# Performance work log

Hardware: AMD Instinct MI355X
Metric: run time of the kernel (lower is better)

The kernel has to match this reference:

```python
import math
import jax, jax.numpy as jnp
import numpy as np

L = 2          # num_layers
B = 2          # micro batch
S = 2048       # seq_length
H = 1024       # hidden_size
NH = 16        # num_attention_heads
DH = 64        # kv_channels (head dim)
FF = 4096      # ffn_hidden_size
EPS = 1e-5
STD = 0.0048


def setup_inputs() -> dict:
    key = jax.random.key(0)
    ks = jax.random.split(key, 12)
    out_std = STD / math.sqrt(2.0 * L)
    # ALiBi slopes for NH=16 (power of 2)
    start = 2.0 ** (-2.0 ** (-(math.log2(NH) - 3)))
    slopes = np.array([start * start ** i for i in range(NH)], dtype=np.float32)
    alibi = slopes[None, :, None, None] * np.arange(S, dtype=np.float32)[None, None, None, :]
    alibi = jnp.asarray(np.broadcast_to(alibi, (B, NH, 1, S)))  # [B, NH, 1, S]
    return {
        "hidden_states": jax.random.normal(ks[0], (B, S, H), jnp.float32),
        "alibi": alibi,
        "qkv_w": jax.random.normal(ks[1], (L, 3 * NH * DH, H), jnp.float32) * STD,
        "qkv_b": jnp.zeros((L, 3 * NH * DH), jnp.float32),
        "dense_w": jax.random.normal(ks[2], (L, H, NH * DH), jnp.float32) * out_std,
        "dense_b": jnp.zeros((L, H), jnp.float32),
        "mlp_w1": jax.random.normal(ks[3], (L, FF, H), jnp.float32) * STD,
        "mlp_b1": jnp.zeros((L, FF), jnp.float32),
        "mlp_w2": jax.random.normal(ks[4], (L, H, FF), jnp.float32) * out_std,
        "mlp_b2": jnp.zeros((L, H), jnp.float32),
        "ln1_w": jnp.ones((L, H), jnp.float32),
        "ln1_b": jnp.zeros((L, H), jnp.float32),
        "ln2_w": jnp.ones((L, H), jnp.float32),
        "ln2_b": jnp.zeros((L, H), jnp.float32),
    }


def _layernorm(x, w, b):
    mu = jnp.mean(x, axis=-1, keepdims=True)
    var = jnp.mean(jnp.square(x - mu), axis=-1, keepdims=True)
    return (x - mu) * jax.lax.rsqrt(var + EPS) * w + b


def _layer(x, alibi, causal, layer_number, qkv_w, qkv_b, dense_w, dense_b,
           mlp_w1, mlp_b1, mlp_w2, mlp_b2, ln1_w, ln1_b, ln2_w, ln2_b):
    # --- attention ---
    h = _layernorm(x, ln1_w, ln1_b)
    qkv = h @ qkv_w.T + qkv_b                       # [B, S, 3*NH*DH]
    q, k, v = jnp.split(qkv, 3, axis=-1)
    q = q.reshape(B, S, NH, DH).transpose(0, 2, 1, 3)  # [B, NH, S, DH]
    k = k.reshape(B, S, NH, DH).transpose(0, 2, 1, 3)
    v = v.reshape(B, S, NH, DH).transpose(0, 2, 1, 3)
    norm_factor = math.sqrt(DH) * layer_number
    beta = 1.0 / layer_number
    alpha = 1.0 / norm_factor
    scores = beta * alibi + alpha * jnp.einsum("bhqd,bhkd->bhqk", q, k)
    # ScaleMaskSoftmax: scale by layer_number, causal mask fill -10000, softmax
    scores = scores * layer_number
    scores = jnp.where(causal, scores, jnp.float32(-10000.0))
    probs = jax.nn.softmax(scores, axis=-1)
    ctx = jnp.einsum("bhqk,bhkd->bhqd", probs, v)   # [B, NH, S, DH]
    ctx = ctx.transpose(0, 2, 1, 3).reshape(B, S, NH * DH)
    attn_out = ctx @ dense_w.T + dense_b
    x = x + attn_out
    # --- MLP ---
    h2 = _layernorm(x, ln2_w, ln2_b)
    m = jax.nn.gelu(h2 @ mlp_w1.T + mlp_b1, approximate=False)
    m = m @ mlp_w2.T + mlp_b2
    return x + m


def reference(hidden_states, alibi, qkv_w, qkv_b, dense_w, dense_b,
              mlp_w1, mlp_b1, mlp_w2, mlp_b2, ln1_w, ln1_b, ln2_w, ln2_b):
    causal = jnp.tril(jnp.ones((S, S), dtype=bool))[None, None]  # [1,1,S,S]
    x = hidden_states
    for l in range(L):
        x = _layer(x, alibi, causal, l + 1,
                   qkv_w[l], qkv_b[l], dense_w[l], dense_b[l],
                   mlp_w1[l], mlp_b1[l], mlp_w2[l], mlp_b2[l],
                   ln1_w[l], ln1_b[l], ln2_w[l], ln2_b[l])
    return x
```

## Files before the change

kernel.cpp:

```cpp
#include <hip/hip_runtime.h>
#include <cstdint>
#include <cmath>

#define SS 2048
#define HH 1024

typedef __bf16 bf16_t;
typedef __bf16 bf16x8 __attribute__((ext_vector_type(8)));
typedef __bf16 bf16x4 __attribute__((ext_vector_type(4)));
typedef float  f32x4  __attribute__((ext_vector_type(4)));

union U32P { unsigned u; bf16_t h[2]; };

__device__ __forceinline__ void async_load16(const void* g, void* l) {
  __builtin_amdgcn_global_load_lds(
      (__attribute__((address_space(1))) void*)(g),
      (__attribute__((address_space(3))) void*)(l), 16, 0, 0);
}

__device__ __forceinline__ void bar_lds() {
  asm volatile("s_waitcnt lgkmcnt(0)" ::: "memory");
  __builtin_amdgcn_s_barrier();
}

__global__ __launch_bounds__(256) void cvt_kernel(const float* __restrict__ in,
                                                  bf16_t* __restrict__ out) {
  size_t i = (size_t)blockIdx.x * 256 + threadIdx.x;
  f32x4 v = ((const f32x4*)in)[i];
  bf16x4 o;
  o[0] = (bf16_t)v[0]; o[1] = (bf16_t)v[1]; o[2] = (bf16_t)v[2]; o[3] = (bf16_t)v[3];
  ((bf16x4*)out)[i] = o;
}

__global__ __launch_bounds__(256) void ln_kernel(const float* __restrict__ x,
                                                 const float* __restrict__ w,
                                                 const float* __restrict__ b,
                                                 bf16_t* __restrict__ out) {
  const int row = blockIdx.x;
  const int tid = threadIdx.x;
  const f32x4 v = ((const f32x4*)(x + (size_t)row * HH))[tid];
  float s  = v[0] + v[1] + v[2] + v[3];
  float s2 = v[0]*v[0] + v[1]*v[1] + v[2]*v[2] + v[3]*v[3];
#pragma unroll
  for (int o = 1; o < 64; o <<= 1) { s += __shfl_xor(s, o); s2 += __shfl_xor(s2, o); }
  __shared__ float r1[4], r2[4];
  if ((tid & 63) == 0) { r1[tid >> 6] = s; r2[tid >> 6] = s2; }
  __syncthreads();
  float ts  = r1[0] + r1[1] + r1[2] + r1[3];
  float ts2 = r2[0] + r2[1] + r2[2] + r2[3];
  float mu  = ts * (1.0f / HH);
  float var = ts2 * (1.0f / HH) - mu * mu;
  float rstd = rsqrtf(var + 1e-5f);
  f32x4 wv = ((const f32x4*)w)[tid];
  f32x4 bv = ((const f32x4*)b)[tid];
  bf16x4 o;
#pragma unroll
  for (int j = 0; j < 4; ++j) o[j] = (bf16_t)((v[j] - mu) * rstd * wv[j] + bv[j]);
  ((bf16x4*)(out + (size_t)row * HH))[tid] = o;
}

__device__ __forceinline__ float gelu_f(float x) {
  return 0.5f * x * (1.0f + erff(x * 0.70710678118654752f));
}

__global__ __launch_bounds__(256) void fuse_add(float* __restrict__ x,
                                                const bf16_t* __restrict__ p0,
                                                const bf16_t* __restrict__ p1,
                                                const float* __restrict__ bias) {
  size_t i = (size_t)blockIdx.x * 256 + threadIdx.x;
  f32x4 xv = ((f32x4*)x)[i];
  bf16x4 a = ((const bf16x4*)p0)[i];
  bf16x4 b4 = ((const bf16x4*)p1)[i];
  f32x4 bv = ((const f32x4*)bias)[i & 255];
#pragma unroll
  for (int j = 0; j < 4; ++j) xv[j] += (float)a[j] + (float)b4[j] + bv[j];
  ((f32x4*)x)[i] = xv;
}

template <int EPI>
__global__ __launch_bounds__(256) void gemm_bt(const bf16_t* __restrict__ A,
                                               const bf16_t* __restrict__ W,
                                               const float* __restrict__ bias,
                                               bf16_t* __restrict__ outb,
                                               int M, int N, int K) {
  __shared__ __align__(16) bf16_t As[128 * 64];
  __shared__ __align__(16) bf16_t Bs[128 * 64];
  const int tid = threadIdx.x;
  const int w = tid >> 6, lane = tid & 63;
  const int m16 = lane & 15, quad = lane >> 4;
  const int wm = w & 1, wn = w >> 1;
  const int n0 = blockIdx.x * 128, m0 = blockIdx.y * 128;

  f32x4 acc[4][4];
#pragma unroll
  for (int i = 0; i < 4; ++i)
#pragma unroll
    for (int j = 0; j < 4; ++j) acc[i][j] = (f32x4){0.f, 0.f, 0.f, 0.f};

  int rowi[4], gci[4];
#pragma unroll
  for (int i = 0; i < 4; ++i) {
    int p = (w * 4 + i) * 64 + lane;
    rowi[i] = p >> 3;
    gci[i] = ((lane & 7) ^ (rowi[i] & 7)) * 8;
  }

  for (int kt = 0; kt < K; kt += 64) {
    __syncthreads();
#pragma unroll
    for (int i = 0; i < 4; ++i) {
      async_load16(A + (size_t)(m0 + rowi[i]) * K + kt + gci[i], &As[(w * 4 + i) * 512]);
      async_load16(W + (size_t)(n0 + rowi[i]) * K + kt + gci[i], &Bs[(w * 4 + i) * 512]);
    }
    __syncthreads();
#pragma unroll
    for (int kk = 0; kk < 2; ++kk) {
      bf16x8 af[4], bfv[4];
#pragma unroll
      for (int mi = 0; mi < 4; ++mi) {
        int row = wm * 64 + mi * 16 + m16;
        int cpos = (kk * 4 + quad) ^ (row & 7);
        af[mi] = *(const bf16x8*)&As[row * 64 + cpos * 8];
      }
#pragma unroll
      for (int ni = 0; ni < 4; ++ni) {
        int row = wn * 64 + ni * 16 + m16;
        int cpos = (kk * 4 + quad) ^ (row & 7);
        bfv[ni] = *(const bf16x8*)&Bs[row * 64 + cpos * 8];
      }
#pragma unroll
      for (int mi = 0; mi < 4; ++mi)
#pragma unroll
        for (int ni = 0; ni < 4; ++ni)
          acc[mi][ni] = __builtin_amdgcn_mfma_f32_16x16x32_bf16(af[mi], bfv[ni],
                                                                acc[mi][ni], 0, 0, 0);
    }
  }

#pragma unroll
  for (int ni = 0; ni < 4; ++ni) {
    int col = n0 + wn * 64 + ni * 16 + m16;
    float bv = bias[col];
#pragma unroll
    for (int mi = 0; mi < 4; ++mi) {
      int rowb = m0 + wm * 64 + mi * 16 + quad * 4;
#pragma unroll
      for (int r = 0; r < 4; ++r) {
        size_t idx = (size_t)(rowb + r) * N + col;
        float v = acc[mi][ni][r] + bv;
        if constexpr (EPI == 1) v = gelu_f(v);
        outb[idx] = (bf16_t)v;
      }
    }
  }
}

__global__ __launch_bounds__(256) void gemm_sk2(const bf16_t* __restrict__ A,
                                                const bf16_t* __restrict__ W,
                                                bf16_t* __restrict__ p0,
                                                bf16_t* __restrict__ p1,
                                                int M, int N, int K) {
  __shared__ __align__(16) bf16_t As[128 * 64];
  __shared__ __align__(16) bf16_t Bs[128 * 64];
  const int tid = threadIdx.x;
  const int w = tid >> 6, lane = tid & 63;
  const int m16 = lane & 15, quad = lane >> 4;
  const int wm = w & 1, wn = w >> 1;
  const int n0 = blockIdx.x * 128, m0 = blockIdx.y * 128;
  const int z = blockIdx.z;
  const int kbeg = z * (K >> 1), kend = kbeg + (K >> 1);
  bf16_t* outb = z ? p1 : p0;

  f32x4 acc[4][4];
#pragma unroll
  for (int i = 0; i < 4; ++i)
#pragma unroll
    for (int j = 0; j < 4; ++j) acc[i][j] = (f32x4){0.f, 0.f, 0.f, 0.f};

  int rowi[4], gci[4];
#pragma unroll
  for (int i = 0; i < 4; ++i) {
    int p = (w * 4 + i) * 64 + lane;
    rowi[i] = p >> 3;
    gci[i] = ((lane & 7) ^ (rowi[i] & 7)) * 8;
  }

  for (int kt = kbeg; kt < kend; kt += 64) {
    __syncthreads();
#pragma unroll
    for (int i = 0; i < 4; ++i) {
      async_load16(A + (size_t)(m0 + rowi[i]) * K + kt + gci[i], &As[(w * 4 + i) * 512]);
      async_load16(W + (size_t)(n0 + rowi[i]) * K + kt + gci[i], &Bs[(w * 4 + i) * 512]);
    }
    __syncthreads();
#pragma unroll
    for (int kk = 0; kk < 2; ++kk) {
      bf16x8 af[4], bfv[4];
#pragma unroll
      for (int mi = 0; mi < 4; ++mi) {
        int row = wm * 64 + mi * 16 + m16;
        int cpos = (kk * 4 + quad) ^ (row & 7);
        af[mi] = *(const bf16x8*)&As[row * 64 + cpos * 8];
      }
#pragma unroll
      for (int ni = 0; ni < 4; ++ni) {
        int row = wn * 64 + ni * 16 + m16;
        int cpos = (kk * 4 + quad) ^ (row & 7);
        bfv[ni] = *(const bf16x8*)&Bs[row * 64 + cpos * 8];
      }
#pragma unroll
      for (int mi = 0; mi < 4; ++mi)
#pragma unroll
        for (int ni = 0; ni < 4; ++ni)
          acc[mi][ni] = __builtin_amdgcn_mfma_f32_16x16x32_bf16(af[mi], bfv[ni],
                                                                acc[mi][ni], 0, 0, 0);
    }
  }

#pragma unroll
  for (int ni = 0; ni < 4; ++ni) {
    int col = n0 + wn * 64 + ni * 16 + m16;
#pragma unroll
    for (int mi = 0; mi < 4; ++mi) {
      int rowb = m0 + wm * 64 + mi * 16 + quad * 4;
#pragma unroll
      for (int r = 0; r < 4; ++r) {
        size_t idx = (size_t)(rowb + r) * N + col;
        outb[idx] = (bf16_t)acc[mi][ni][r];
      }
    }
  }
}

__global__ __launch_bounds__(256) void attn_kernel(const bf16_t* __restrict__ qkv,
                                                   bf16_t* __restrict__ ctx,
                                                   bf16_t* __restrict__ pa0,
                                                   float* __restrict__ pl0,
                                                   bf16_t* __restrict__ pa1,
                                                   float* __restrict__ pl1) {
  const int qt = 31 - blockIdx.y;
  const int bh = blockIdx.x;
  const int b = bh >> 4, h = bh & 15;
  const int tid = threadIdx.x;
  const int w = tid >> 6, lane = tid & 63;
  const int m16 = lane & 15, quad = lane >> 4;

  const float slope2 = __builtin_amdgcn_exp2f(-0.70710678118654752f * (float)(h + 1))
                       * 1.4426950408889634f;
  const int wt = (int)((30.0f / slope2 + 63.0f) * 0.015625f);
  const int kt0 = (qt - wt > 0) ? (qt - wt) : 0;
  const int nch = (qt - kt0 + 8) >> 3;
  const int z = blockIdx.z;
  if (z >= nch) return;
  const int ktb = kt0 + z * 8;
  const int kte = (ktb + 7 < qt) ? (ktb + 7) : qt;
  const bool multi = (nch > 1);

  __shared__ __align__(16) bf16_t Vt[2][64 * 72];
  __shared__ __align__(16) bf16_t Pl[4][16 * 72];

  const int q_abs = qt * 64 + w * 16 + m16;
  float alkb[16];
#pragma unroll
  for (int kn = 0; kn < 4; ++kn)
#pragma unroll
    for (int r = 0; r < 4; ++r)
      alkb[kn * 4 + r] = slope2 * (float)(ktb * 64 + kn * 16 + quad * 4 + r - q_abs);
  const float d64 = slope2 * 64.0f;

  const int qrow = qt * 64 + w * 16 + m16;
  const bf16_t* qbase = qkv + (size_t)(b * SS + qrow) * 3072 + h * 64;
  const bf16x8 bq0 = *(const bf16x8*)(qbase + quad * 8);
  const bf16x8 bq1 = *(const bf16x8*)(qbase + 32 + quad * 8);

  const bf16_t* kbase = qkv + (size_t)(b * SS + m16) * 3072 + 1024 + h * 64 + quad * 8;
  const int kp2 = (tid & 31) * 2, vd0 = (tid >> 5) * 8;
  const bf16_t* vsrc = qkv + (size_t)(b * SS + kp2) * 3072 + 2048 + h * 64 + vd0;
  const int ql = w * 16 + m16;
  constexpr float C = 0.18033688011112042f;

  f32x4 acc[4];
#pragma unroll
  for (int i = 0; i < 4; ++i) acc[i] = (f32x4){0.f, 0.f, 0.f, 0.f};
  float rs_l = 0.f;

  bf16x8 ak[4][2], v0, v1;
  {
    const bf16_t* kb = kbase + (size_t)ktb * 64 * 3072;
#pragma unroll
    for (int kn = 0; kn < 4; ++kn) {
      ak[kn][0] = *(const bf16x8*)(kb + (size_t)(kn * 16) * 3072);
      ak[kn][1] = *(const bf16x8*)(kb + (size_t)(kn * 16) * 3072 + 32);
    }
    const bf16_t* vs = vsrc + (size_t)ktb * 64 * 3072;
    v0 = *(const bf16x8*)(vs);
    v1 = *(const bf16x8*)(vs + 3072);
  }
#pragma unroll
  for (int j = 0; j < 8; ++j) {
    U32P pk; pk.h[0] = v0[j]; pk.h[1] = v1[j];
    *(unsigned*)&Vt[ktb & 1][(vd0 + j) * 72 + kp2] = pk.u;
  }

  for (int kt = ktb; kt <= kte; ++kt) {
    bar_lds();

    bf16x8 nk[4][2], nv0 = v0, nv1 = v1;
    if (kt < kte) {
      const bf16_t* kb = kbase + (size_t)(kt + 1) * 64 * 3072;
#pragma unroll
      for (int kn = 0; kn < 4; ++kn) {
        nk[kn][0] = *(const bf16x8*)(kb + (size_t)(kn * 16) * 3072);
        nk[kn][1] = *(const bf16x8*)(kb + (size_t)(kn * 16) * 3072 + 32);
      }
      const bf16_t* nsrc = vsrc + (size_t)(kt + 1) * 64 * 3072;
      nv0 = *(const bf16x8*)(nsrc);
      nv1 = *(const bf16x8*)(nsrc + 3072);
    } else {
#pragma unroll
      for (int kn = 0; kn < 4; ++kn) { nk[kn][0] = ak[kn][0]; nk[kn][1] = ak[kn][1]; }
    }

    __builtin_amdgcn_s_setprio(1);
    float p[16];
    const bool diag = (kt == qt);
#pragma unroll
    for (int kn = 0; kn < 4; ++kn) {
      f32x4 zz = (f32x4){0.f, 0.f, 0.f, 0.f};
      zz = __builtin_amdgcn_mfma_f32_16x16x32_bf16(ak[kn][0], bq0, zz, 0, 0, 0);
      zz = __builtin_amdgcn_mfma_f32_16x16x32_bf16(ak[kn][1], bq1, zz, 0, 0, 0);
#pragma unroll
      for (int r = 0; r < 4; ++r) {
        float s = fmaf(zz[r], C, alkb[kn * 4 + r]);
        if (diag) {
          int kl = kn * 16 + quad * 4 + r;
          if (kl > ql) s = -INFINITY;
        }
        float e = __builtin_amdgcn_exp2f(s);
        p[kn * 4 + r] = e;
        rs_l += e;
      }
    }
#pragma unroll
    for (int i = 0; i < 16; ++i) alkb[i] += d64;

#pragma unroll
    for (int kn = 0; kn < 4; ++kn) {
      U32P a, c;
      a.h[0] = (bf16_t)p[kn * 4 + 0]; a.h[1] = (bf16_t)p[kn * 4 + 1];
      c.h[0] = (bf16_t)p[kn * 4 + 2]; c.h[1] = (bf16_t)p[kn * 4 + 3];
      uint2 pk; pk.x = a.u; pk.y = c.u;
      *(uint2*)&Pl[w][m16 * 72 + kn * 16 + quad * 4] = pk;
    }
    const bf16_t* vt = &Vt[kt & 1][0];
    bf16x8 bp0 = *(const bf16x8*)&Pl[w][m16 * 72 + quad * 8];
    bf16x8 bp1 = *(const bf16x8*)&Pl[w][m16 * 72 + 32 + quad * 8];
#pragma unroll
    for (int ni = 0; ni < 4; ++ni) {
      bf16x8 av0 = *(const bf16x8*)&vt[(ni * 16 + m16) * 72 + quad * 8];
      bf16x8 av1 = *(const bf16x8*)&vt[(ni * 16 + m16) * 72 + 32 + quad * 8];
      acc[ni] = __builtin_amdgcn_mfma_f32_16x16x32_bf16(av0, bp0, acc[ni], 0, 0, 0);
      acc[ni] = __builtin_amdgcn_mfma_f32_16x16x32_bf16(av1, bp1, acc[ni], 0, 0, 0);
    }
    __builtin_amdgcn_s_setprio(0);

    if (kt < kte) {
#pragma unroll
      for (int j = 0; j < 8; ++j) {
        U32P pk; pk.h[0] = nv0[j]; pk.h[1] = nv1[j];
        *(unsigned*)&Vt[(kt + 1) & 1][(vd0 + j) * 72 + kp2] = pk.u;
      }
    }
#pragma unroll
    for (int kn = 0; kn < 4; ++kn) { ak[kn][0] = nk[kn][0]; ak[kn][1] = nk[kn][1]; }
    v0 = nv0; v1 = nv1;
  }

  rs_l += __shfl_xor(rs_l, 16);
  rs_l += __shfl_xor(rs_l, 32);

  if (!multi) {
    const float inv_l = 1.0f / rs_l;
    bf16_t* cb = ctx + (size_t)(b * SS + qt * 64 + w * 16 + m16) * 1024 + h * 64;
#pragma unroll
    for (int ni = 0; ni < 4; ++ni) {
      U32P a, c;
      a.h[0] = (bf16_t)(acc[ni][0] * inv_l); a.h[1] = (bf16_t)(acc[ni][1] * inv_l);
      c.h[0] = (bf16_t)(acc[ni][2] * inv_l); c.h[1] = (bf16_t)(acc[ni][3] * inv_l);
      uint2 pk; pk.x = a.u; pk.y = c.u;
      *(uint2*)(cb + ni * 16 + quad * 4) = pk;
    }
  } else {
    const int sl = (h - 6) * 24 + (qt - 8);
    bf16_t* ab = (b ? pa1 : pa0) + (size_t)(sl * 4 + z) * 4096
                 + (size_t)(w * 16 + m16) * 64;
#pragma unroll
    for (int ni = 0; ni < 4; ++ni) {
      U32P a, c;
      a.h[0] = (bf16_t)acc[ni][0]; a.h[1] = (bf16_t)acc[ni][1];
      c.h[0] = (bf16_t)acc[ni][2]; c.h[1] = (bf16_t)acc[ni][3];
      uint2 pk; pk.x = a.u; pk.y = c.u;
      *(uint2*)(ab + ni * 16 + quad * 4) = pk;
    }
    if (quad == 0) (b ? pl1 : pl0)[(sl * 4 + z) * 64 + w * 16 + m16] = rs_l;
  }
}

__global__ __launch_bounds__(256) void attn_norm(const bf16_t* __restrict__ pa0,
                                                 const float* __restrict__ pl0,
                                                 const bf16_t* __restrict__ pa1,
                                                 const float* __restrict__ pl1,
                                                 bf16_t* __restrict__ ctx) {
  const int gs = blockIdx.x;
  const int b = gs >= 240, sl = b ? gs - 240 : gs;
  const int h = sl / 24 + 6, qt = sl % 24 + 8;
  const bf16_t* pa = b ? pa1 : pa0;
  const float* pl = b ? pl1 : pl0;
  const float slope2 = __builtin_amdgcn_exp2f(-0.70710678118654752f * (float)(h + 1))
                       * 1.4426950408889634f;
  const int wt = (int)((30.0f / slope2 + 63.0f) * 0.015625f);
  const int kt0 = (qt - wt > 0) ? (qt - wt) : 0;
  const int nch = (qt - kt0 + 8) >> 3;

  const int t = threadIdx.x;
  const int q = t >> 2, d0 = (t & 3) << 4;
  const bf16_t* ap = pa + (size_t)sl * 4 * 4096 + (size_t)q * 64 + d0;
  float av[16];
#pragma unroll
  for (int j = 0; j < 16; ++j) av[j] = 0.f;
  float l = 0.f;
  for (int z = 0; z < nch; ++z) {
    bf16x8 a0 = *(const bf16x8*)(ap + (size_t)z * 4096);
    bf16x8 a1 = *(const bf16x8*)(ap + (size_t)z * 4096 + 8);
#pragma unroll
    for (int j = 0; j < 8; ++j) { av[j] += (float)a0[j]; av[8 + j] += (float)a1[j]; }
    l += pl[(sl * 4 + z) * 64 + q];
  }
  const float invl = 1.0f / l;
  bf16_t* cp = ctx + (size_t)(b * SS + qt * 64 + q) * 1024 + h * 64 + d0;
  bf16x8 o0, o1;
#pragma unroll
  for (int j = 0; j < 8; ++j) o0[j] = (bf16_t)(av[j] * invl);
#pragma unroll
  for (int j = 0; j < 8; ++j) o1[j] = (bf16_t)(av[8 + j] * invl);
  *(bf16x8*)cp = o0;
  *(bf16x8*)(cp + 8) = o1;
}

extern "C" void kernel_launch(void* const* d_in, const int* in_sizes, int n_in,
                              void* d_out, int out_size, void* d_ws, size_t ws_size,
                              hipStream_t stream) {
  const float* hs    = (const float*)d_in[0];
  const float* qkvw  = (const float*)d_in[2];
  const float* qkvb  = (const float*)d_in[3];
  const float* dw    = (const float*)d_in[4];
  const float* db    = (const float*)d_in[5];
  const float* w1    = (const float*)d_in[6];
  const float* b1    = (const float*)d_in[7];
  const float* w2    = (const float*)d_in[8];
  const float* b2    = (const float*)d_in[9];
  const float* ln1w  = (const float*)d_in[10];
  const float* ln1b  = (const float*)d_in[11];
  const float* ln2w  = (const float*)d_in[12];
  const float* ln2b  = (const float*)d_in[13];
  float* x = (float*)d_out;

  char* ws = (char*)d_ws;
  bf16_t* wqc = (bf16_t*)(ws + 0);
  bf16_t* wdc = (bf16_t*)(ws + 12582912);
  bf16_t* w1c = (bf16_t*)(ws + 16777216);
  bf16_t* w2c = (bf16_t*)(ws + 33554432);
  bf16_t* hb  = (bf16_t*)(ws + 50331648);
  bf16_t* qm  = (bf16_t*)(ws + 58720256);
  bf16_t* cx  = (bf16_t*)(ws + 92274688);
  bf16_t* dp0 = qm;
  bf16_t* dp1 = qm + (size_t)4096 * 1024;
  bf16_t* pa0 = (bf16_t*)(ws + 50331648);
  float*  pl0 = (float*)(ws + 50331648 + (size_t)240 * 4 * 4096 * 2);
  bf16_t* pa1 = (bf16_t*)(ws + 83886080);
  float*  pl1 = (float*)(ws + 83886080 + (size_t)240 * 4 * 4096 * 2);

  hipMemcpyAsync(x, hs, (size_t)4096 * 1024 * 4, hipMemcpyDeviceToDevice, stream);
  cvt_kernel<<<6144, 256, 0, stream>>>(qkvw, wqc);
  cvt_kernel<<<2048, 256, 0, stream>>>(dw, wdc);
  cvt_kernel<<<8192, 256, 0, stream>>>(w1, w1c);
  cvt_kernel<<<8192, 256, 0, stream>>>(w2, w2c);

  for (int l = 0; l < 2; ++l) {
    ln_kernel<<<4096, 256, 0, stream>>>(x, ln1w + l * 1024, ln1b + l * 1024, hb);
    gemm_bt<0><<<dim3(24, 32), 256, 0, stream>>>(hb, wqc + (size_t)l * 3145728,
        qkvb + l * 3072, qm, 4096, 3072, 1024);
    attn_kernel<<<dim3(32, 32, 4), 256, 0, stream>>>(qm, cx, pa0, pl0, pa1, pl1);
    attn_norm<<<480, 256, 0, stream>>>(pa0, pl0, pa1, pl1, cx);
    gemm_sk2<<<dim3(8, 32, 2), 256, 0, stream>>>(cx, wdc + (size_t)l * 1048576,
        dp0, dp1, 4096, 1024, 1024);
    fuse_add<<<4096, 256, 0, stream>>>(x, dp0, dp1, db + l * 1024);
    ln_kernel<<<4096, 256, 0, stream>>>(x, ln2w + l * 1024, ln2b + l * 1024, hb);
    gemm_bt<1><<<dim3(32, 32), 256, 0, stream>>>(hb, w1c + (size_t)l * 4194304,
        b1 + l * 4096, qm, 4096, 4096, 1024);
    gemm_sk2<<<dim3(8, 32, 2), 256, 0, stream>>>(qm, w2c + (size_t)l * 4194304,
        hb, cx, 4096, 1024, 4096);
    fuse_add<<<4096, 256, 0, stream>>>(x, hb, cx, b2 + l * 1024);
  }
}
```

Before: 718.0 us.

## Write K and V in head-major layout from QKV GEMM for attention

Adds a dedicated QKV GEMM whose epilogue scatters Q into a compact [B,S,1024] buffer and K/V into contiguous per-head [B,NH,S,64] buffers. The attention kernel then reads K and V tiles from contiguous 128-byte rows instead of rows strided by 3072 elements. The aim is better cache-line and TLB locality for the attention K/V stream. In exchange the GEMM epilogue issues scattered 2-byte stores, and the new buffers must not overlap the split-K partial buffers.

Result: slower. 744.5 us (+3.7%).

```diff
diff --git a/kernel.cpp b/kernel.cpp
--- a/kernel.cpp
+++ b/kernel.cpp
@@ -150,6 +150,92 @@
         float v = acc[mi][ni][r] + bv;
         if constexpr (EPI == 1) v = gelu_f(v);
         outb[idx] = (bf16_t)v;
+      }
+    }
+  }
+}
+
+__global__ __launch_bounds__(256) void gemm_qkv(const bf16_t* __restrict__ A,
+                                                const bf16_t* __restrict__ W,
+                                                const float* __restrict__ bias,
+                                                bf16_t* __restrict__ qc,
+                                                bf16_t* __restrict__ kc,
+                                                bf16_t* __restrict__ vc) {
+  const int M = 4096, N = 3072, K = 1024;
+  __shared__ __align__(16) bf16_t As[128 * 64];
+  __shared__ __align__(16) bf16_t Bs[128 * 64];
+  const int tid = threadIdx.x;
+  const int w = tid >> 6, lane = tid & 63;
+  const int m16 = lane & 15, quad = lane >> 4;
+  const int wm = w & 1, wn = w >> 1;
+  const int n0 = blockIdx.x * 128, m0 = blockIdx.y * 128;
+
+  f32x4 acc[4][4];
+#pragma unroll
+  for (int i = 0; i < 4; ++i)
+#pragma unroll
+    for (int j = 0; j < 4; ++j) acc[i][j] = (f32x4){0.f, 0.f, 0.f, 0.f};
+
+  int rowi[4], gci[4];
+#pragma unroll
+  for (int i = 0; i < 4; ++i) {
+    int p = (w * 4 + i) * 64 + lane;
+    rowi[i] = p >> 3;
+    gci[i] = ((lane & 7) ^ (rowi[i] & 7)) * 8;
+  }
+
+  for (int kt = 0; kt < K; kt += 64) {
+    __syncthreads();
+#pragma unroll
+    for (int i = 0; i < 4; ++i) {
+      async_load16(A + (size_t)(m0 + rowi[i]) * K + kt + gci[i], &As[(w * 4 + i) * 512]);
+      async_load16(W + (size_t)(n0 + rowi[i]) * K + kt + gci[i], &Bs[(w * 4 + i) * 512]);
+    }
+    __syncthreads();
+#pragma unroll
+    for (int kk = 0; kk < 2; ++kk) {
+      bf16x8 af[4], bfv[4];
+#pragma unroll
+      for (int mi = 0; mi < 4; ++mi) {
+        int row = wm * 64 + mi * 16 + m16;
+        int cpos = (kk * 4 + quad) ^ (row & 7);
+        af[mi] = *(const bf16x8*)&As[row * 64 + cpos * 8];
+      }
+#pragma unroll
+      for (int ni = 0; ni < 4; ++ni) {
+        int row = wn * 64 + ni * 16 + m16;
+        int cpos = (kk * 4 + quad) ^ (row & 7);
+        bfv[ni] = *(const bf16x8*)&Bs[row * 64 + cpos * 8];
+      }
+#pragma unroll
+      for (int mi = 0; mi < 4; ++mi)
+#pragma unroll
+        for (int ni = 0; ni < 4; ++ni)
+          acc[mi][ni] = __builtin_amdgcn_mfma_f32_16x16x32_bf16(af[mi], bfv[ni],
+                                                                acc[mi][ni], 0, 0, 0);
+    }
+  }
+
+  const int bb = m0 >> 11;
+  const int sbase = (m0 & 2047) + wm * 64;
+#pragma unroll
+  for (int ni = 0; ni < 4; ++ni) {
+    int col = n0 + wn * 64 + ni * 16 + m16;
+    float bv = bias[col];
+    int region = col >> 10;
+    int h = (col >> 6) & 15, d = col & 63;
+#pragma unroll
+    for (int mi = 0; mi < 4; ++mi) {
+#pragma unroll
+      for (int r = 0; r < 4; ++r) {
+        int s = sbase + mi * 16 + quad * 4 + r;
+        float v = acc[mi][ni][r] + bv;
+        if (region == 0) {
+          qc[(size_t)(bb * SS + s) * 1024 + col] = (bf16_t)v;
+        } else {
+          bf16_t* o = (region == 1) ? kc : vc;
+          o[((size_t)(bb * 16 + h) * SS + s) * 64 + d] = (bf16_t)v;
+        }
       }
     }
   }
@@ -232,7 +318,9 @@
   }
 }
 
-__global__ __launch_bounds__(256) void attn_kernel(const bf16_t* __restrict__ qkv,
+__global__ __launch_bounds__(256) void attn_kernel(const bf16_t* __restrict__ qc,
+                                                   const bf16_t* __restrict__ kc,
+                                                   const bf16_t* __restrict__ vcp,
                                                    bf16_t* __restrict__ ctx,
                                                    bf16_t* __restrict__ pa0,
                                                    float* __restrict__ pl0,
@@ -269,13 +357,13 @@
   const float d64 = slope2 * 64.0f;
 
   const int qrow = qt * 64 + w * 16 + m16;
-  const bf16_t* qbase = qkv + (size_t)(b * SS + qrow) * 3072 + h * 64;
+  const bf16_t* qbase = qc + (size_t)(b * SS + qrow) * 1024 + h * 64;
   const bf16x8 bq0 = *(const bf16x8*)(qbase + quad * 8);
   const bf16x8 bq1 = *(const bf16x8*)(qbase + 32 + quad * 8);
 
-  const bf16_t* kbase = qkv + (size_t)(b * SS + m16) * 3072 + 1024 + h * 64 + quad * 8;
+  const bf16_t* kbase = kc + ((size_t)(b * 16 + h) * SS + m16) * 64 + quad * 8;
   const int kp2 = (tid & 31) * 2, vd0 = (tid >> 5) * 8;
-  const bf16_t* vsrc = qkv + (size_t)(b * SS + kp2) * 3072 + 2048 + h * 64 + vd0;
+  const bf16_t* vsrc = vcp + ((size_t)(b * 16 + h) * SS + kp2) * 64 + vd0;
   const int ql = w * 16 + m16;
   constexpr float C = 0.18033688011112042f;
 
@@ -286,15 +374,15 @@
 
   bf16x8 ak[4][2], v0, v1;
   {
-    const bf16_t* kb = kbase + (size_t)ktb * 64 * 3072;
+    const bf16_t* kb = kbase + (size_t)ktb * 4096;
 #pragma unroll
     for (int kn = 0; kn < 4; ++kn) {
-      ak[kn][0] = *(const bf16x8*)(kb + (size_t)(kn * 16) * 3072);
-      ak[kn][1] = *(const bf16x8*)(kb + (size_t)(kn * 16) * 3072 + 32);
-    }
-    const bf16_t* vs = vsrc + (size_t)ktb * 64 * 3072;
+      ak[kn][0] = *(const bf16x8*)(kb + kn * 1024);
+      ak[kn][1] = *(const bf16x8*)(kb + kn * 1024 + 32);
+    }
+    const bf16_t* vs = vsrc + (size_t)ktb * 4096;
     v0 = *(const bf16x8*)(vs);
-    v1 = *(const bf16x8*)(vs + 3072);
+    v1 = *(const bf16x8*)(vs + 64);
   }
 #pragma unroll
   for (int j = 0; j < 8; ++j) {
@@ -307,15 +395,15 @@
 
     bf16x8 nk[4][2], nv0 = v0, nv1 = v1;
     if (kt < kte) {
-      const bf16_t* kb = kbase + (size_t)(kt + 1) * 64 * 3072;
+      const bf16_t* kb = kbase + (size_t)(kt + 1) * 4096;
 #pragma unroll
       for (int kn = 0; kn < 4; ++kn) {
-        nk[kn][0] = *(const bf16x8*)(kb + (size_t)(kn * 16) * 3072);
-        nk[kn][1] = *(const bf16x8*)(kb + (size_t)(kn * 16) * 3072 + 32);
-      }
-      const bf16_t* nsrc = vsrc + (size_t)(kt + 1) * 64 * 3072;
+        nk[kn][0] = *(const bf16x8*)(kb + kn * 1024);
+        nk[kn][1] = *(const bf16x8*)(kb + kn * 1024 + 32);
+      }
+      const bf16_t* nsrc = vsrc + (size_t)(kt + 1) * 4096;
       nv0 = *(const bf16x8*)(nsrc);
-      nv1 = *(const bf16x8*)(nsrc + 3072);
+      nv1 = *(const bf16x8*)(nsrc + 64);
     } else {
 #pragma unroll
       for (int kn = 0; kn < 4; ++kn) { nk[kn][0] = ak[kn][0]; nk[kn][1] = ak[kn][1]; }
@@ -473,6 +561,9 @@
   bf16_t* hb  = (bf16_t*)(ws + 50331648);
   bf16_t* qm  = (bf16_t*)(ws + 58720256);
   bf16_t* cx  = (bf16_t*)(ws + 92274688);
+  bf16_t* qc = (bf16_t*)(ws + 58720256);
+  bf16_t* kc = (bf16_t*)(ws + 67108864);
+  bf16_t* vc = (bf16_t*)(ws + 75497472);
   bf16_t* dp0 = qm;
   bf16_t* dp1 = qm + (size_t)4096 * 1024;
   bf16_t* pa0 = (bf16_t*)(ws + 50331648);
@@ -488,9 +579,10 @@
 
   for (int l = 0; l < 2; ++l) {
     ln_kernel<<<4096, 256, 0, stream>>>(x, ln1w + l * 1024, ln1b + l * 1024, hb);
-    gemm_bt<0><<<dim3(24, 32), 256, 0, stream>>>(hb, wqc + (size_t)l * 3145728,
-        qkvb + l * 3072, qm, 4096, 3072, 1024);
-    attn_kernel<<<dim3(32, 32, 4), 256, 0, stream>>>(qm, cx, pa0, pl0, pa1, pl1);
+    gemm_qkv<<<dim3(24, 32), 256, 0, stream>>>(hb, wqc + (size_t)l * 3145728,
+        qkvb + l * 3072, qc, kc, vc);
+    attn_kernel<<<dim3(32, 32, 4), 256, 0, stream>>>(qc, kc, vc, cx,
+        pa0, pl0, pa1, pl1);
     attn_norm<<<480, 256, 0, stream>>>(pa0, pl0, pa1, pl1, cx);
     gemm_sk2<<<dim3(8, 32, 2), 256, 0, stream>>>(cx, wdc + (size_t)l * 1048576,
         dp0, dp1, 4096, 1024, 1024);
```
